# Performance work log

Hardware: AMD Instinct MI355X
Metric: run time of the kernel (lower is better)

## Reference

```python
import jax, jax.numpy as jnp
import numpy as np

N_SENS, N_HID, N_MOT = 10000, 400000, 1000
E_SH, E_HH, E_HM = 4_000_000, 16_000_000, 400_000
BETA, THR, SLOPE = 0.9, 1.0, 25.0  # snn.Leaky(beta, threshold), surrogate.fast_sigmoid(slope=25)

# Heaviside spike with fast-sigmoid surrogate gradient (matches snnTorch)
@jax.custom_vjp
def spike(x):
    return (x > 0).astype(x.dtype)

def _spike_fwd(x):
    return (x > 0).astype(x.dtype), x

def _spike_bwd(x, g):
    return (g / (SLOPE * jnp.abs(x) + 1.0) ** 2,)

spike.defvjp(_spike_fwd, _spike_bwd)

def lif(inp, mem):
    # snn.Leaky, reset_mechanism='zero': mem = beta*mem + I; spike; reset to 0 where spiked
    mem = BETA * mem + inp
    spk = spike(mem - THR)
    mem = mem - jax.lax.stop_gradient(spk) * mem  # reset detached, as in snnTorch
    return spk, mem

def spmm_t(pre_idx, post_idx, w, pre_spikes, n_post):
    # torch.sparse.mm(W^T, pre_spikes): gather pre activity along edges, scatter-add to post
    contrib = w * pre_spikes[pre_idx]          # [E]
    return jax.ops.segment_sum(contrib, post_idx, num_segments=n_post)

def setup_inputs() -> dict:
    key = jax.random.key(0)
    ks = jax.random.split(key, 16)
    std_sh = 1.0 / np.sqrt(N_SENS * 0.001)
    std_hh = 1.0 / np.sqrt(N_HID * 0.0001)
    std_hm = 1.0 / np.sqrt(N_HID * 0.001)
    return {
        "sensory_input": jax.random.uniform(ks[0], (N_SENS,), jnp.float32),
        "sensory_mem": jax.random.uniform(ks[1], (N_SENS,), jnp.float32),
        "hidden_mem": jax.random.uniform(ks[2], (N_HID,), jnp.float32),
        "motor_mem": jax.random.uniform(ks[3], (N_MOT,), jnp.float32),
        "hidden_prev_spikes": (jax.random.uniform(ks[4], (N_HID,)) < 0.05).astype(jnp.float32),
        "w_sh": jax.random.normal(ks[5], (E_SH,), jnp.float32) * std_sh,
        "w_hh": jax.random.normal(ks[6], (E_HH,), jnp.float32) * std_hh,
        "w_hm": jax.random.normal(ks[7], (E_HM,), jnp.float32) * std_hm,
        "sh_pre": jax.random.randint(ks[8], (E_SH,), 0, N_SENS, jnp.int32),
        "sh_post": jax.random.randint(ks[9], (E_SH,), 0, N_HID, jnp.int32),
        "hh_pre": jax.random.randint(ks[10], (E_HH,), 0, N_HID, jnp.int32),
        "hh_post": jax.random.randint(ks[11], (E_HH,), 0, N_HID, jnp.int32),
        "hm_pre": jax.random.randint(ks[12], (E_HM,), 0, N_HID, jnp.int32),
        "hm_post": jax.random.randint(ks[13], (E_HM,), 0, N_MOT, jnp.int32),
    }

def reference(sensory_input, sensory_mem, hidden_mem, motor_mem, hidden_prev_spikes,
              w_sh, w_hh, w_hm, sh_pre, sh_post, hh_pre, hh_post, hm_pre, hm_post):
    sens_spk, _ = lif(sensory_input * 5.0, sensory_mem)
    hid_in = spmm_t(sh_pre, sh_post, w_sh, sens_spk, N_HID)
    hid_in = hid_in + 0.5 * spmm_t(hh_pre, hh_post, w_hh, hidden_prev_spikes, N_HID)
    hid_spk, _ = lif(hid_in * 5.0, hidden_mem)
    mot_in = spmm_t(hm_pre, hm_post, w_hm, hid_spk, N_MOT)
    mot_spk, _ = lif(mot_in * 20.0, motor_mem)
    return mot_spk
```

## Files before the change

### kernel.cpp

```cpp
#include <hip/hip_runtime.h>


#define N_SENS 10000
#define N_HID  400000
#define N_MOT  1000

#define CHUNK_LOG 14
#define CHUNK     (1 << CHUNK_LOG)
#define NBUCKET   25
#define CAP       196608
#define NCOPY     10

#define SENS_MW   320
#define HID_MW    12512

#define EPT_SH    8
#define BUF_SH    8192
#define EPT_HH    32
#define BUF_HH    2048

#define NB_HM     64

__global__ void make_masks(const float* __restrict__ sens_in,
                           const float* __restrict__ sens_mem,
                           const float* __restrict__ hid_prev,
                           uint2* __restrict__ smask,
                           uint2* __restrict__ hmask,
                           float* __restrict__ extra,
                           int* __restrict__ cursors, int nb_sens) {
    bool pred = false;
    int i;
    uint2* dst;
    int maxw;
    if ((int)blockIdx.x < nb_sens) {
        if (blockIdx.x == 0 && threadIdx.x < 32) cursors[threadIdx.x] = 0;
        i = blockIdx.x * blockDim.x + threadIdx.x;
        if (i < N_SENS) pred = (0.9f * sens_mem[i] + 5.0f * sens_in[i]) > 1.0f;
        dst = smask; maxw = SENS_MW / 2;
    } else {
        i = (blockIdx.x - nb_sens) * blockDim.x + threadIdx.x;
        if (i < N_HID) { pred = (hid_prev[i] != 0.0f); extra[i] = 0.0f; }
        dst = hmask; maxw = HID_MW / 2;
    }
    unsigned long long b = __ballot(pred);
    if ((threadIdx.x & 63) == 0) {
        int w = i >> 6;
        if (w < maxw) dst[w] = make_uint2((unsigned)b, (unsigned)(b >> 32));
    }
}

template <int MW, int BUFCAP, int EPT>
__global__ __launch_bounds__(1024, 8)
void bin_scan(const int* __restrict__ pre, const int* __restrict__ post,
              const float* __restrict__ w, const unsigned* __restrict__ gmask,
              int n_e, float scale,
              uint2* __restrict__ pairs, int* __restrict__ gcursor,
              float* __restrict__ extra) {
    __shared__ unsigned sm[MW];
    __shared__ uint2 buf[BUFCAP];
    __shared__ int h[4][32];
    __shared__ int gb[32];
    __shared__ int lcur[32];
    __shared__ int total;

    const int tid = threadIdx.x;
    const int lane = tid & 63;
    for (int i = tid; i < MW / 4; i += 1024)
        ((uint4*)sm)[i] = ((const uint4*)gmask)[i];
    if (tid < 128) ((int*)h)[tid] = 0;
    if (tid == 0) total = 0;
    __syncthreads();

    const int base = blockIdx.x * (1024 * EPT) + tid;

    unsigned am = 0;
    #pragma unroll
    for (int j = 0; j < EPT; ++j) {
        int e = base + j * 1024;
        if (e < n_e) {
            int pr = pre[e];
            if ((sm[pr >> 5] >> (pr & 31)) & 1u) am |= (1u << j);
        }
    }
    int cnt = __popc(am);

    int inc = cnt;
    #pragma unroll
    for (int d = 1; d < 64; d <<= 1) {
        int n = __shfl_up(inc, d);
        if (lane >= d) inc += n;
    }
    int wtot = __shfl(inc, 63);
    int wbase = 0;
    if (lane == 63 && wtot) wbase = atomicAdd(&total, wtot);
    wbase = __shfl(wbase, 63);
    int off = wbase + inc - cnt;

    #pragma unroll
    for (int j = 0; j < EPT; ++j) {
        if ((am >> j) & 1u) {
            int e = base + j * 1024;
            unsigned p = (unsigned)post[e];
            float wv = scale * w[e];
            if (off < BUFCAP) buf[off] = make_uint2(p, __float_as_uint(wv));
            else atomicAdd(&extra[p], wv);
            ++off;
        }
    }
    __syncthreads();
    int tot = total; if (tot > BUFCAP) tot = BUFCAP;

    int rep = (tid >> 6) & 3;
    for (int k = tid; k < tot; k += 1024)
        atomicAdd(&h[rep][buf[k].x >> CHUNK_LOG], 1);
    __syncthreads();
    if (tid < NBUCKET) {
        int hb = h[0][tid] + h[1][tid] + h[2][tid] + h[3][tid];
        gb[tid] = hb ? atomicAdd(&gcursor[tid], hb) : 0;
        lcur[tid] = 0;
    }
    __syncthreads();

    for (int k = tid; k < tot; k += 1024) {
        uint2 u = buf[k];
        int b = u.x >> CHUNK_LOG;
        int s = atomicAdd(&lcur[b], 1);
        int pos = gb[b] + s;
        if (pos < CAP)
            pairs[(size_t)b * CAP + pos] =
                make_uint2(u.x & (CHUNK - 1), u.y);
        else
            atomicAdd(&extra[u.x], __uint_as_float(u.y));
    }
}

__global__ __launch_bounds__(1024, 8)
void accum_bucket(const uint2* __restrict__ pairs,
                  const int* __restrict__ cursors,
                  float* __restrict__ partials) {
    int bucket = blockIdx.x / NCOPY;
    int copy   = blockIdx.x % NCOPY;
    __shared__ float acc[CHUNK];
    for (int i = threadIdx.x; i < CHUNK; i += blockDim.x) acc[i] = 0.0f;
    __syncthreads();

    int count = cursors[bucket];
    if (count > CAP) count = CAP;
    int begin = (int)((long long)count * copy / NCOPY);
    int end   = (int)((long long)count * (copy + 1) / NCOPY);
    const uint2* src = pairs + (size_t)bucket * CAP;
    for (int i = begin + threadIdx.x; i < end; i += blockDim.x) {
        uint2 u = src[i];
        atomicAdd(&acc[u.x], __uint_as_float(u.y));
    }
    __syncthreads();
    float* dst = partials + ((size_t)bucket * NCOPY + copy) * CHUNK;
    for (int i = threadIdx.x; i < CHUNK; i += blockDim.x) dst[i] = acc[i];
}

__global__ void reduce_lif_hidden_mask(const float* __restrict__ partials,
                                       const float* __restrict__ extra,
                                       const float* __restrict__ mem,
                                       uint2* __restrict__ mask) {
    int i = blockIdx.x * blockDim.x + threadIdx.x;
    bool pred = false;
    if (i < N_HID) {
        int b = i >> CHUNK_LOG, local = i & (CHUNK - 1);
        const float* p = partials + (size_t)b * NCOPY * CHUNK + local;
        float sum = extra[i];
        #pragma unroll
        for (int c = 0; c < NCOPY; ++c) sum += p[(size_t)c * CHUNK];
        pred = (0.9f * mem[i] + 5.0f * sum) > 1.0f;
    }
    unsigned long long bal = __ballot(pred);
    if ((threadIdx.x & 63) == 0) {
        int w = i >> 6;
        if (w < HID_MW / 2)
            mask[w] = make_uint2((unsigned)bal, (unsigned)(bal >> 32));
    }
}

__global__ __launch_bounds__(1024, 8)
void scatter_motor_mask(const int* __restrict__ pre,
                        const int* __restrict__ post,
                        const float* __restrict__ w,
                        const unsigned* __restrict__ gmask,
                        float* __restrict__ partials, int n_edges) {
    __shared__ float acc[N_MOT];
    __shared__ unsigned sm[HID_MW];
    for (int i = threadIdx.x; i < HID_MW / 4; i += blockDim.x)
        ((uint4*)sm)[i] = ((const uint4*)gmask)[i];
    for (int j = threadIdx.x; j < N_MOT; j += blockDim.x) acc[j] = 0.0f;
    __syncthreads();
    for (int e = blockIdx.x * blockDim.x + threadIdx.x; e < n_edges;
         e += gridDim.x * blockDim.x) {
        int pr = pre[e];
        if ((sm[pr >> 5] >> (pr & 31)) & 1u)
            atomicAdd(&acc[post[e]], w[e]);
    }
    __syncthreads();
    float* out = partials + (size_t)blockIdx.x * N_MOT;
    for (int j = threadIdx.x; j < N_MOT; j += blockDim.x) out[j] = acc[j];
}

__global__ void reduce_lif_motor(const float* __restrict__ partials, int nb,
                                 const float* __restrict__ mem,
                                 float* __restrict__ out) {
    int m = blockIdx.x * blockDim.x + threadIdx.x;
    if (m >= N_MOT) return;
    float sum = 0.0f;
    for (int b = 0; b < nb; ++b) sum += partials[(size_t)b * N_MOT + m];
    float v = 0.9f * mem[m] + 20.0f * sum;
    out[m] = (v > 1.0f) ? 1.0f : 0.0f;
}

__global__ void lif_kernel(const float* __restrict__ inp,
                           const float* __restrict__ mem_in,
                           float* __restrict__ spk,
                           float scale, int n) {
    int i = blockIdx.x * blockDim.x + threadIdx.x;
    if (i < n) {
        float m = 0.9f * mem_in[i] + scale * inp[i];
        spk[i] = (m > 1.0f) ? 1.0f : 0.0f;
    }
}

__global__ void scatter_dev(const int* __restrict__ pre,
                            const int* __restrict__ post,
                            const float* __restrict__ w,
                            const float* __restrict__ spikes,
                            float* __restrict__ out,
                            float scale, int n_edges) {
    int e = blockIdx.x * blockDim.x + threadIdx.x;
    if (e >= n_edges) return;
    float s = spikes[pre[e]];
    if (s != 0.0f) atomicAdd(&out[post[e]], scale * w[e] * s);
}

__global__ void lif_hidden_direct(const float* __restrict__ hid_in,
                                  const float* __restrict__ mem,
                                  float* __restrict__ spk) {
    int i = blockIdx.x * blockDim.x + threadIdx.x;
    if (i >= N_HID) return;
    float m = 0.9f * mem[i] + 5.0f * hid_in[i];
    spk[i] = (m > 1.0f) ? 1.0f : 0.0f;
}

__global__ void scatter_motor_f(const int* __restrict__ pre,
                                const int* __restrict__ post,
                                const float* __restrict__ w,
                                const float* __restrict__ spikes,
                                float* __restrict__ partials, int n_edges) {
    __shared__ float acc[N_MOT];
    for (int j = threadIdx.x; j < N_MOT; j += blockDim.x) acc[j] = 0.0f;
    __syncthreads();
    for (int e = blockIdx.x * blockDim.x + threadIdx.x; e < n_edges;
         e += gridDim.x * blockDim.x) {
        float s = spikes[pre[e]];
        if (s != 0.0f) atomicAdd(&acc[post[e]], w[e] * s);
    }
    __syncthreads();
    float* out = partials + (size_t)blockIdx.x * N_MOT;
    for (int j = threadIdx.x; j < N_MOT; j += blockDim.x) out[j] = acc[j];
}

extern "C" void kernel_launch(void* const* d_in, const int* in_sizes, int n_in,
                              void* d_out, int out_size, void* d_ws, size_t ws_size,
                              hipStream_t stream) {
    const float* sensory_input = (const float*)d_in[0];
    const float* sensory_mem   = (const float*)d_in[1];
    const float* hidden_mem    = (const float*)d_in[2];
    const float* motor_mem     = (const float*)d_in[3];
    const float* hidden_prev   = (const float*)d_in[4];
    const float* w_sh          = (const float*)d_in[5];
    const float* w_hh          = (const float*)d_in[6];
    const float* w_hm          = (const float*)d_in[7];
    const int*   sh_pre        = (const int*)d_in[8];
    const int*   sh_post       = (const int*)d_in[9];
    const int*   hh_pre        = (const int*)d_in[10];
    const int*   hh_post       = (const int*)d_in[11];
    const int*   hm_pre        = (const int*)d_in[12];
    const int*   hm_post       = (const int*)d_in[13];
    const int e_sh = in_sizes[5];
    const int e_hh = in_sizes[6];
    const int e_hm = in_sizes[7];
    const int B = 256;

    size_t o_cursor = 0;
    size_t o_extra  = 32;
    size_t o_pairs  = o_extra + N_HID;
    size_t o_part   = o_pairs + (size_t)NBUCKET * CAP * 2;
    size_t o_smask  = o_part + (size_t)NBUCKET * NCOPY * CHUNK;
    size_t o_hmaskp = o_smask + SENS_MW;
    size_t o_hmasks = o_hmaskp + HID_MW;
    size_t o_mpart  = o_hmasks + HID_MW;
    size_t f_need   = o_mpart + (size_t)NB_HM * N_MOT;
    bool fast = (ws_size / sizeof(float)) >= f_need;

    float* ws = (float*)d_ws;
    if (fast) {
        int*      cursors = (int*)(ws + o_cursor);
        float*    extra   = ws + o_extra;
        uint2*    pairs   = (uint2*)(ws + o_pairs);
        float*    part    = ws + o_part;
        unsigned* smask   = (unsigned*)(ws + o_smask);
        unsigned* hmaskp  = (unsigned*)(ws + o_hmaskp);
        unsigned* hmasks  = (unsigned*)(ws + o_hmasks);
        float*    mpart   = ws + o_mpart;

        int nb_sens = (N_SENS + B - 1) / B;
        int nb_hidm = (N_HID + B - 1) / B;
        make_masks<<<nb_sens + nb_hidm, B, 0, stream>>>(
            sensory_input, sensory_mem, hidden_prev,
            (uint2*)smask, (uint2*)hmaskp, extra, cursors, nb_sens);

        int nb_sh = (e_sh + 1024 * EPT_SH - 1) / (1024 * EPT_SH);
        int nb_hh = (e_hh + 1024 * EPT_HH - 1) / (1024 * EPT_HH);
        bin_scan<SENS_MW, BUF_SH, EPT_SH><<<nb_sh, 1024, 0, stream>>>(
            sh_pre, sh_post, w_sh, smask, e_sh, 1.0f, pairs, cursors, extra);
        bin_scan<HID_MW, BUF_HH, EPT_HH><<<nb_hh, 1024, 0, stream>>>(
            hh_pre, hh_post, w_hh, hmaskp, e_hh, 0.5f, pairs, cursors, extra);

        accum_bucket<<<NBUCKET * NCOPY, 1024, 0, stream>>>(pairs, cursors, part);
        reduce_lif_hidden_mask<<<(N_HID + B - 1) / B, B, 0, stream>>>(
            part, extra, hidden_mem, (uint2*)hmasks);
        scatter_motor_mask<<<NB_HM, 1024, 0, stream>>>(
            hm_pre, hm_post, w_hm, hmasks, mpart, e_hm);
        reduce_lif_motor<<<(N_MOT + B - 1) / B, B, 0, stream>>>(
            mpart, NB_HM, motor_mem, (float*)d_out);
    } else {
        float* hid_in   = ws;
        float* sens_spk = hid_in + N_HID;
        float* hid_spk  = sens_spk + 10016;
        float* mpart    = hid_spk + N_HID;
        hipMemsetAsync(hid_in, 0, (size_t)N_HID * sizeof(float), stream);
        lif_kernel<<<(N_SENS + B - 1) / B, B, 0, stream>>>(
            sensory_input, sensory_mem, sens_spk, 5.0f, N_SENS);
        scatter_dev<<<(e_sh + B - 1) / B, B, 0, stream>>>(
            sh_pre, sh_post, w_sh, sens_spk, hid_in, 1.0f, e_sh);
        scatter_dev<<<(e_hh + B - 1) / B, B, 0, stream>>>(
            hh_pre, hh_post, w_hh, hidden_prev, hid_in, 0.5f, e_hh);
        lif_hidden_direct<<<(N_HID + B - 1) / B, B, 0, stream>>>(
            hid_in, hidden_mem, hid_spk);
        scatter_motor_f<<<NB_HM, B, 0, stream>>>(
            hm_pre, hm_post, w_hm, hid_spk, mpart, e_hm);
        reduce_lif_motor<<<(N_MOT + B - 1) / B, B, 0, stream>>>(
            mpart, NB_HM, motor_mem, (float*)d_out);
    }
}
```

Baseline: 338.2 us.

## Merge two edge-binning kernels into one interleaved launch with vectorized loads

Replaces the two separate bin_scan launches (sensory-to-hidden and hidden-to-hidden) with a single bin_stream kernel whose blocks alternate between the two edge sets and share one dynamically partitioned shared-memory region. Edge pre/post/weight arrays are now read as int4/float4 vectors, four edges per thread per group. Compaction uses per-wave ballots with an atomic on the block total, and the bucket histogram is updated during the scan instead of in a separate pass. The aim is to cut one launch plus its tail, use memory bandwidth better, and remove a shared-memory pass. The cost is more shared atomics per ballot step and a buffer order that is no longer grouped per thread.

```diff
diff --git a/kernel.cpp b/kernel.cpp
--- a/kernel.cpp
+++ b/kernel.cpp
@@ -14,10 +14,12 @@
 #define SENS_MW   320
 #define HID_MW    12512
 
-#define EPT_SH    8
+#define G_SH      2
 #define BUF_SH    8192
-#define EPT_HH    32
+#define G_HH      8
 #define BUF_HH    2048
+
+#define SMEM_BYTES 66816
 
 #define NB_HM     64
 
@@ -49,71 +51,112 @@
     }
 }
 
-template <int MW, int BUFCAP, int EPT>
+template <int G, int BUFCAP>
+__device__ __forceinline__
+void bin_body(const int* __restrict__ pre, const int* __restrict__ post,
+              const float* __restrict__ w, int n_e, float scale,
+              const unsigned* sm, uint2* buf, int (*h)[32], int* total,
+              float* __restrict__ extra, int blockStart) {
+    const int tid = threadIdx.x;
+    const int lane = tid & 63;
+    const unsigned long long lt = (1ull << lane) - 1ull;
+    const int rep = (tid >> 6) & 3;
+    const int base4 = (blockStart >> 2) + tid;
+    #pragma unroll
+    for (int g = 0; g < G; ++g) {
+        int e4 = base4 + g * 1024;
+        int e0 = e4 << 2;
+        int4 pr4 = make_int4(-1, -1, -1, -1);
+        int4 po4 = make_int4(0, 0, 0, 0);
+        float4 wv4 = make_float4(0.f, 0.f, 0.f, 0.f);
+        if (e0 + 3 < n_e) {
+            pr4 = ((const int4*)pre)[e4];
+            po4 = ((const int4*)post)[e4];
+            wv4 = ((const float4*)w)[e4];
+        } else if (e0 < n_e) {
+            int t[4] = {-1, -1, -1, -1}, q[4] = {0, 0, 0, 0};
+            float f[4] = {0.f, 0.f, 0.f, 0.f};
+            for (int k = 0; k < 4; ++k) {
+                int e = e0 + k;
+                if (e < n_e) { t[k] = pre[e]; q[k] = post[e]; f[k] = w[e]; }
+            }
+            pr4 = make_int4(t[0], t[1], t[2], t[3]);
+            po4 = make_int4(q[0], q[1], q[2], q[3]);
+            wv4 = make_float4(f[0], f[1], f[2], f[3]);
+        }
+        int   prk[4] = {pr4.x, pr4.y, pr4.z, pr4.w};
+        int   pok[4] = {po4.x, po4.y, po4.z, po4.w};
+        float wk[4]  = {wv4.x, wv4.y, wv4.z, wv4.w};
+        #pragma unroll
+        for (int k = 0; k < 4; ++k) {
+            int pr = prk[k];
+            bool act = (pr >= 0) && ((sm[pr >> 5] >> (pr & 31)) & 1u);
+            unsigned long long m = __ballot(act);
+            if (!m) continue;
+            int bse = 0;
+            if (lane == 0) bse = atomicAdd(total, (int)__popcll(m));
+            bse = __shfl(bse, 0);
+            if (act) {
+                int idx = bse + (int)__popcll(m & lt);
+                unsigned p = (unsigned)pok[k];
+                float wv = scale * wk[k];
+                if (idx < BUFCAP) {
+                    buf[idx] = make_uint2(p, __float_as_uint(wv));
+                    atomicAdd(&h[rep][p >> CHUNK_LOG], 1);
+                } else {
+                    atomicAdd(&extra[p], wv);
+                }
+            }
+        }
+    }
+}
+
 __global__ __launch_bounds__(1024, 8)
-void bin_scan(const int* __restrict__ pre, const int* __restrict__ post,
-              const float* __restrict__ w, const unsigned* __restrict__ gmask,
-              int n_e, float scale,
-              uint2* __restrict__ pairs, int* __restrict__ gcursor,
-              float* __restrict__ extra) {
-    __shared__ unsigned sm[MW];
-    __shared__ uint2 buf[BUFCAP];
+void bin_stream(const int* __restrict__ sh_pre, const int* __restrict__ sh_post,
+                const float* __restrict__ w_sh, const unsigned* __restrict__ smask,
+                int e_sh, int nb_sh,
+                const int* __restrict__ hh_pre, const int* __restrict__ hh_post,
+                const float* __restrict__ w_hh, const unsigned* __restrict__ hmask,
+                int e_hh, int nb_hh,
+                uint2* __restrict__ pairs, int* __restrict__ gcursor,
+                float* __restrict__ extra) {
+    __shared__ __align__(16) char smem[SMEM_BYTES];
     __shared__ int h[4][32];
     __shared__ int gb[32];
     __shared__ int lcur[32];
     __shared__ int total;
 
     const int tid = threadIdx.x;
-    const int lane = tid & 63;
-    for (int i = tid; i < MW / 4; i += 1024)
-        ((uint4*)sm)[i] = ((const uint4*)gmask)[i];
+    const int bid = blockIdx.x;
+
+    int nmin = (nb_sh < nb_hh) ? nb_sh : nb_hh;
+    bool is_sh;
+    int idx;
+    if (bid < 2 * nmin) { is_sh = ((bid & 1) == 0); idx = bid >> 1; }
+    else { is_sh = (nb_sh > nb_hh); idx = bid - 2 * nmin + nmin; }
+
+    const unsigned* gm = is_sh ? smask : hmask;
+    const int mw = is_sh ? SENS_MW : HID_MW;
+    unsigned* sm = (unsigned*)smem;
+    uint2* buf = (uint2*)(smem + (size_t)mw * 4);
+
     if (tid < 128) ((int*)h)[tid] = 0;
     if (tid == 0) total = 0;
-    __syncthreads();
-
-    const int base = blockIdx.x * (1024 * EPT) + tid;
-
-    unsigned am = 0;
-    #pragma unroll
-    for (int j = 0; j < EPT; ++j) {
-        int e = base + j * 1024;
-        if (e < n_e) {
-            int pr = pre[e];
-            if ((sm[pr >> 5] >> (pr & 31)) & 1u) am |= (1u << j);
-        }
-    }
-    int cnt = __popc(am);
-
-    int inc = cnt;
-    #pragma unroll
-    for (int d = 1; d < 64; d <<= 1) {
-        int n = __shfl_up(inc, d);
-        if (lane >= d) inc += n;
-    }
-    int wtot = __shfl(inc, 63);
-    int wbase = 0;
-    if (lane == 63 && wtot) wbase = atomicAdd(&total, wtot);
-    wbase = __shfl(wbase, 63);
-    int off = wbase + inc - cnt;
-
-    #pragma unroll
-    for (int j = 0; j < EPT; ++j) {
-        if ((am >> j) & 1u) {
-            int e = base + j * 1024;
-            unsigned p = (unsigned)post[e];
-            float wv = scale * w[e];
-            if (off < BUFCAP) buf[off] = make_uint2(p, __float_as_uint(wv));
-            else atomicAdd(&extra[p], wv);
-            ++off;
-        }
-    }
-    __syncthreads();
-    int tot = total; if (tot > BUFCAP) tot = BUFCAP;
-
-    int rep = (tid >> 6) & 3;
-    for (int k = tid; k < tot; k += 1024)
-        atomicAdd(&h[rep][buf[k].x >> CHUNK_LOG], 1);
-    __syncthreads();
+    for (int i = tid; i < mw / 4; i += 1024)
+        ((uint4*)sm)[i] = ((const uint4*)gm)[i];
+    __syncthreads();
+
+    if (is_sh)
+        bin_body<G_SH, BUF_SH>(sh_pre, sh_post, w_sh, e_sh, 1.0f,
+                               sm, buf, h, &total, extra, idx * (4096 * G_SH));
+    else
+        bin_body<G_HH, BUF_HH>(hh_pre, hh_post, w_hh, e_hh, 0.5f,
+                               sm, buf, h, &total, extra, idx * (4096 * G_HH));
+    __syncthreads();
+
+    int bufcap = is_sh ? BUF_SH : BUF_HH;
+    int tot = total; if (tot > bufcap) tot = bufcap;
+
     if (tid < NBUCKET) {
         int hb = h[0][tid] + h[1][tid] + h[2][tid] + h[3][tid];
         gb[tid] = hb ? atomicAdd(&gcursor[tid], hb) : 0;
@@ -314,12 +357,12 @@
             sensory_input, sensory_mem, hidden_prev,
             (uint2*)smask, (uint2*)hmaskp, extra, cursors, nb_sens);
 
-        int nb_sh = (e_sh + 1024 * EPT_SH - 1) / (1024 * EPT_SH);
-        int nb_hh = (e_hh + 1024 * EPT_HH - 1) / (1024 * EPT_HH);
-        bin_scan<SENS_MW, BUF_SH, EPT_SH><<<nb_sh, 1024, 0, stream>>>(
-            sh_pre, sh_post, w_sh, smask, e_sh, 1.0f, pairs, cursors, extra);
-        bin_scan<HID_MW, BUF_HH, EPT_HH><<<nb_hh, 1024, 0, stream>>>(
-            hh_pre, hh_post, w_hh, hmaskp, e_hh, 0.5f, pairs, cursors, extra);
+        int nb_sh = (e_sh + 4096 * G_SH - 1) / (4096 * G_SH);
+        int nb_hh = (e_hh + 4096 * G_HH - 1) / (4096 * G_HH);
+        bin_stream<<<nb_sh + nb_hh, 1024, 0, stream>>>(
+            sh_pre, sh_post, w_sh, smask, e_sh, nb_sh,
+            hh_pre, hh_post, w_hh, hmaskp, e_hh, nb_hh,
+            pairs, cursors, extra);
 
         accum_bucket<<<NBUCKET * NCOPY, 1024, 0, stream>>>(pairs, cursors, part);
         reduce_lif_hidden_mask<<<(N_HID + B - 1) / B, B, 0, stream>>>(
```

After: 326.8 us. -3.4%, faster.
